# Optimization experiments

Hardware: AMD Instinct MI355X
Metric: run time of the kernel (lower is better)

## Reference

```python
import math
import jax, jax.numpy as jnp
import numpy as np

B, S, D, H = 2, 2048, 1024, 16
HD = D // H  # head_dim = 64
LN_EPS = 1e-5


def setup_inputs() -> dict:
    key = jax.random.key(0)
    ks = jax.random.split(key, 12)
    scale = 1.0 / math.sqrt(D)
    inp = {
        "x": jax.random.normal(ks[0], (B, S, D), dtype=jnp.float32),
        "cdr_mask": jax.random.uniform(ks[1], (B, 1, S, S), dtype=jnp.float32),
        "Wq": jax.random.normal(ks[2], (D, D), dtype=jnp.float32) * scale,
        "bq": jnp.zeros((D,), dtype=jnp.float32),
        "Wk": jax.random.normal(ks[3], (D, D), dtype=jnp.float32) * scale,
        "bk": jnp.zeros((D,), dtype=jnp.float32),
        "Wv": jax.random.normal(ks[4], (D, D), dtype=jnp.float32) * scale,
        "bv": jnp.zeros((D,), dtype=jnp.float32),
        "Wo": jax.random.normal(ks[5], (D, D), dtype=jnp.float32) * scale,
        "bo": jnp.zeros((D,), dtype=jnp.float32),
        "gamma": jnp.ones((D,), dtype=jnp.float32),
        "beta": jnp.zeros((D,), dtype=jnp.float32),
        "cdr_weight": jnp.float32(1.0),
    }
    return inp


def _rotate_half(t):
    # even / odd interleaved halves, as in the torch module
    t1 = t[..., ::2]
    t2 = t[..., 1::2]
    return jnp.stack((-t2, t1), axis=-1).reshape(t.shape)


def reference(x, cdr_mask, Wq, bq, Wk, bk, Wv, bv, Wo, bo, gamma, beta, cdr_weight):
    b, s, d = x.shape
    # RoPE tables (concatenated, NOT interleaved -- faithful to source)
    inv_freq = 1.0 / (10000.0 ** (jnp.arange(0, HD, 2, dtype=jnp.float32) / HD))
    pos = jnp.arange(s, dtype=jnp.float32)
    sinusoid = pos[:, None] * inv_freq[None, :]          # [S, HD/2]
    sin_pos = jnp.concatenate([jnp.sin(sinusoid)] * 2, axis=-1)[None, None]  # [1,1,S,HD]
    cos_pos = jnp.concatenate([jnp.cos(sinusoid)] * 2, axis=-1)[None, None]

    def proj(W, bias):
        return (x @ W.T + bias).reshape(b, s, H, HD).transpose(0, 2, 1, 3)  # [B,H,S,HD]

    Q = proj(Wq, bq)
    K = proj(Wk, bk)
    V = proj(Wv, bv)
    Q = Q * cos_pos + _rotate_half(Q) * sin_pos
    K = K * cos_pos + _rotate_half(K) * sin_pos

    scores = jnp.einsum('bhqd,bhkd->bhqk', Q, K) / math.sqrt(HD)
    scores = scores + cdr_mask * cdr_weight
    probs = jax.nn.softmax(scores, axis=-1)
    attn = jnp.einsum('bhqk,bhkd->bhqd', probs, V)       # [B,H,S,HD]
    attn = attn.transpose(0, 2, 1, 3).reshape(b, s, d)
    out = attn @ Wo.T + bo                               # dropout is identity at eval

    y = x + out
    mu = jnp.mean(y, axis=-1, keepdims=True)
    var = jnp.var(y, axis=-1, keepdims=True)
    return (y - mu) / jnp.sqrt(var + LN_EPS) * gamma + beta
```

## Files before the change

### kernel.cpp

```cpp
#include <hip/hip_runtime.h>
#include <hip/hip_bf16.h>
#include <math.h>

#define Bn  2
#define Sn  2048
#define Dn  1024
#define Hn  16
#define HDn 64

typedef __attribute__((ext_vector_type(8))) short bf16x8;
typedef __attribute__((ext_vector_type(4))) short bf16x4;
typedef __attribute__((ext_vector_type(4))) float f32x4;

#define LOG2E 1.44269504088896340736f

__device__ __forceinline__ float fexp2(float x) {
    return __builtin_amdgcn_exp2f(x);
}

__device__ __forceinline__ uint2 pack4bf(float a, float b, float c, float d) {
    union { __hip_bfloat162 h2[2]; uint2 u; } p;
    p.h2[0] = __float22bfloat162_rn(make_float2(a, b));
    p.h2[1] = __float22bfloat162_rn(make_float2(c, d));
    return p.u;
}

__device__ __forceinline__ bf16x4 pack4bfv(float a, float b, float c, float d) {
    union { __hip_bfloat162 h2[2]; bf16x4 v; } p;
    p.h2[0] = __float22bfloat162_rn(make_float2(a, b));
    p.h2[1] = __float22bfloat162_rn(make_float2(c, d));
    return p.v;
}

__device__ __forceinline__ void g2l16(const void* g, void* lbase) {
    __builtin_amdgcn_global_load_lds(
        (const __attribute__((address_space(1))) void*)g,
        (__attribute__((address_space(3))) void*)lbase, 16, 0, 0);
}

__global__ __launch_bounds__(256) void prep_kernel(
    const float* __restrict__ x,
    const float* __restrict__ Wq, const float* __restrict__ Wk,
    const float* __restrict__ Wv, const float* __restrict__ Wo,
    __hip_bfloat16* __restrict__ Xb,
    __hip_bfloat16* __restrict__ Wqb, __hip_bfloat16* __restrict__ Wkb,
    __hip_bfloat16* __restrict__ Wvb, __hip_bfloat16* __restrict__ Wob)
{
    const int bx = blockIdx.x, tid = threadIdx.x;
    if (bx < 4096) {
        const size_t i = (size_t)bx * 1024 + tid * 4;
        float4 v = *(const float4*)(x + i);
        *(uint2*)(Xb + i) = pack4bf(v.x, v.y, v.z, v.w);
    } else {
        const int r = bx - 4096;
        const int which = r >> 10;
        const size_t i = (size_t)(r & 1023) * 1024 + tid * 4;
        const float* s = (which == 0) ? Wq : (which == 1) ? Wk : (which == 2) ? Wv : Wo;
        __hip_bfloat16* d = (which == 0) ? Wqb : (which == 1) ? Wkb : (which == 2) ? Wvb : Wob;
        float4 v = *(const float4*)(s + i);
        *(uint2*)(d + i) = pack4bf(v.x, v.y, v.z, v.w);
    }
}

__global__ __launch_bounds__(256) void qkv_proj(
    const __hip_bfloat16* __restrict__ X,
    const __hip_bfloat16* __restrict__ Wqb, const __hip_bfloat16* __restrict__ Wkb,
    const __hip_bfloat16* __restrict__ Wvb,
    const float* __restrict__ bq, const float* __restrict__ bk,
    const float* __restrict__ bv,
    __hip_bfloat16* __restrict__ Qo, __hip_bfloat16* __restrict__ Ko,
    __hip_bfloat16* __restrict__ Vo)
{
    __shared__ __hip_bfloat16 Xs[128 * 32];
    __shared__ __hip_bfloat16 Ws[128 * 32];
    const int tid  = threadIdx.x;
    const int w    = tid >> 6, lane = tid & 63;
    const int lrow = lane & 15, lhi = lane >> 4;
    const int L    = blockIdx.x;
    const int xcd  = L & 7, slot = L >> 3;
    const int wq   = slot >> 2, ms = slot & 3;
    const int pj   = wq >> 3;
    const int n0   = (wq & 7) * 128;
    const int m0   = (xcd + 8 * ms) * 128;
    const int rm   = (w & 1) * 64;
    const int rn   = (w >> 1) * 64;
    const int srow = lane >> 2, cb = lane & 3;

    const __hip_bfloat16* Wb   = (pj == 0) ? Wqb : (pj == 1) ? Wkb : Wvb;
    const float*          bias = (pj == 0) ? bq : (pj == 1) ? bk : bv;

    f32x4 acc[16];
#pragma unroll
    for (int i = 0; i < 16; i++) acc[i] = (f32x4){0.f, 0.f, 0.f, 0.f};

    for (int k0 = 0; k0 < Dn; k0 += 32) {
#pragma unroll
        for (int j = 0; j < 2; j++) {
            const int row = w * 32 + j * 16 + srow;
            const int sc  = (cb ^ ((row >> 1) & 3)) << 3;
            g2l16(X  + (size_t)(m0 + row) * Dn + k0 + sc, &Xs[(w * 32 + j * 16) * 32]);
            g2l16(Wb + (size_t)(n0 + row) * Dn + k0 + sc, &Ws[(w * 32 + j * 16) * 32]);
        }
        __syncthreads();

        bf16x8 FX[4], FW[4];
#pragma unroll
        for (int t = 0; t < 4; t++) {
            const int ra = rm + t * 16 + lrow;
            FX[t] = *(const bf16x8*)&Xs[ra * 32 + ((lhi ^ ((ra >> 1) & 3)) << 3)];
            const int rb = rn + t * 16 + lrow;
            FW[t] = *(const bf16x8*)&Ws[rb * 32 + ((lhi ^ ((rb >> 1) & 3)) << 3)];
        }
        if (pj == 2) {
#pragma unroll
            for (int tm = 0; tm < 4; tm++)
#pragma unroll
                for (int tn = 0; tn < 4; tn++)
                    acc[tm * 4 + tn] = __builtin_amdgcn_mfma_f32_16x16x32_bf16(
                        FX[tm], FW[tn], acc[tm * 4 + tn], 0, 0, 0);
        } else {
#pragma unroll
            for (int tn = 0; tn < 4; tn++)
#pragma unroll
                for (int tm = 0; tm < 4; tm++)
                    acc[tn * 4 + tm] = __builtin_amdgcn_mfma_f32_16x16x32_bf16(
                        FW[tn], FX[tm], acc[tn * 4 + tm], 0, 0, 0);
        }
        __syncthreads();
    }

    const int h = (n0 >> 6) + (w >> 1);

    if (pj != 2) {
        __hip_bfloat16* outb = (pj == 0) ? Qo : Ko;
        const float NEG_L2C = -0.41524101186092033f;
        const float SCL = 0.125f * LOG2E;
#pragma unroll
        for (int tn = 0; tn < 4; tn++) {
            const int hd0 = tn * 16 + lhi * 4;
            const float4 b4 = *(const float4*)&bias[n0 + rn + hd0];
            const float f0 = exp2f((float)((hd0 + 0) & 31) * NEG_L2C);
            const float f1 = exp2f((float)((hd0 + 1) & 31) * NEG_L2C);
            const float f2 = exp2f((float)((hd0 + 2) & 31) * NEG_L2C);
            const float f3 = exp2f((float)((hd0 + 3) & 31) * NEG_L2C);
#pragma unroll
            for (int tm = 0; tm < 4; tm++) {
                const int m = m0 + rm + tm * 16 + lrow;
                const int s = m & (Sn - 1), bb = m >> 11;
                f32x4 a = acc[tn * 4 + tm];
                float v0 = a[0] + b4.x, v1 = a[1] + b4.y;
                float v2 = a[2] + b4.z, v3 = a[3] + b4.w;
                if (pj == 0) { v0 *= SCL; v1 *= SCL; v2 *= SCL; v3 *= SCL; }
                const float sf = (float)s;
                const float c0 = __cosf(sf * f0), c1 = __cosf(sf * f1);
                const float c2 = __cosf(sf * f2), c3 = __cosf(sf * f3);
                const float s0 = __sinf(sf * f0), s1 = __sinf(sf * f1);
                const float s2 = __sinf(sf * f2), s3 = __sinf(sf * f3);
                const float r0 = v0 * c0 - v1 * s0;
                const float r1 = v1 * c1 + v0 * s1;
                const float r2 = v2 * c2 - v3 * s2;
                const float r3 = v3 * c3 + v2 * s3;
                *(uint2*)(outb + ((size_t)(bb * Hn + h) * Sn + s) * HDn + hd0) =
                    pack4bf(r0, r1, r2, r3);
            }
        }
    } else {
#pragma unroll
        for (int tn = 0; tn < 4; tn++) {
            const int c = tn * 16 + lrow;
            const float bc = bias[n0 + rn + c];
#pragma unroll
            for (int tm = 0; tm < 4; tm++) {
                const int mb = m0 + rm + tm * 16 + lhi * 4;
                const int s = mb & (Sn - 1), bb = mb >> 11;
                f32x4 a = acc[tm * 4 + tn];
                *(uint2*)(Vo + ((size_t)(bb * Hn + h) * HDn + c) * Sn + s) =
                    pack4bf(a[0] + bc, a[1] + bc, a[2] + bc, a[3] + bc);
            }
        }
    }
}

__global__ __launch_bounds__(256) void o_proj(
    const __hip_bfloat16* __restrict__ X,
    const __hip_bfloat16* __restrict__ Wb,
    const float* __restrict__ bias,
    const float* __restrict__ resid,
    float* __restrict__ outf)
{
    __shared__ __hip_bfloat16 Xs[128 * 32];
    __shared__ __hip_bfloat16 Ws[128 * 32];
    const int tid  = threadIdx.x;
    const int w    = tid >> 6, lane = tid & 63;
    const int lrow = lane & 15, lhi = lane >> 4;
    const int L    = blockIdx.x;
    const int xcd  = L & 7, slot = L >> 3;
    const int n0   = (slot >> 2) * 128;
    const int m0   = (xcd + 8 * (slot & 3)) * 128;
    const int rm   = (w & 1) * 64;
    const int rn   = (w >> 1) * 64;
    const int srow = lane >> 2, cb = lane & 3;

    f32x4 acc[16];
#pragma unroll
    for (int i = 0; i < 16; i++) acc[i] = (f32x4){0.f, 0.f, 0.f, 0.f};

    for (int k0 = 0; k0 < Dn; k0 += 32) {
#pragma unroll
        for (int j = 0; j < 2; j++) {
            const int row = w * 32 + j * 16 + srow;
            const int sc  = (cb ^ ((row >> 1) & 3)) << 3;
            g2l16(X  + (size_t)(m0 + row) * Dn + k0 + sc, &Xs[(w * 32 + j * 16) * 32]);
            g2l16(Wb + (size_t)(n0 + row) * Dn + k0 + sc, &Ws[(w * 32 + j * 16) * 32]);
        }
        __syncthreads();

        bf16x8 FX[4], FW[4];
#pragma unroll
        for (int t = 0; t < 4; t++) {
            const int ra = rm + t * 16 + lrow;
            FX[t] = *(const bf16x8*)&Xs[ra * 32 + ((lhi ^ ((ra >> 1) & 3)) << 3)];
            const int rb = rn + t * 16 + lrow;
            FW[t] = *(const bf16x8*)&Ws[rb * 32 + ((lhi ^ ((rb >> 1) & 3)) << 3)];
        }
#pragma unroll
        for (int tn = 0; tn < 4; tn++)
#pragma unroll
            for (int tm = 0; tm < 4; tm++)
                acc[tn * 4 + tm] = __builtin_amdgcn_mfma_f32_16x16x32_bf16(
                    FW[tn], FX[tm], acc[tn * 4 + tm], 0, 0, 0);
        __syncthreads();
    }

#pragma unroll
    for (int tn = 0; tn < 4; tn++) {
        const int nb = n0 + rn + tn * 16 + lhi * 4;
        const float4 b4 = *(const float4*)&bias[nb];
#pragma unroll
        for (int tm = 0; tm < 4; tm++) {
            const int m = m0 + rm + tm * 16 + lrow;
            f32x4 a = acc[tn * 4 + tm];
            const float4 rr = *(const float4*)&resid[(size_t)m * Dn + nb];
            *(float4*)(outf + (size_t)m * Dn + nb) =
                make_float4(a[0] + b4.x + rr.x, a[1] + b4.y + rr.y,
                            a[2] + b4.z + rr.z, a[3] + b4.w + rr.w);
        }
    }
}

struct __align__(16) TileBuf {
    __hip_bfloat16 K[64 * 64];
    __hip_bfloat16 V[64 * 64];
    float          M[64 * 64];
};

__device__ __forceinline__ void stage_tiles(
    TileBuf& t,
    const __hip_bfloat16* __restrict__ Kb,
    const __hip_bfloat16* __restrict__ Vb,
    const float* __restrict__ Mq0,
    int k0, int w, int lane)
{
#pragma unroll
    for (int j = 0; j < 2; j++) {
        const int row = w * 16 + j * 8 + (lane >> 3);
        const int blk = (lane & 7) ^ (row & 7);
        g2l16(Kb + (size_t)(k0 + row) * HDn + blk * 8, &t.K[(w * 16 + j * 8) * 64]);
        g2l16(Vb + (size_t)row * Sn + k0 + blk * 8,    &t.V[(w * 16 + j * 8) * 64]);
    }
#pragma unroll
    for (int j = 0; j < 4; j++) {
        const int row = w * 16 + j * 4 + (lane >> 4);
        const int blk = (lane & 15) ^ (row & 7);
        g2l16(Mq0 + (size_t)row * Sn + k0 + blk * 4,   &t.M[(w * 16 + j * 4) * 64]);
    }
}

__global__ __launch_bounds__(256) void attn_kernel(
    const __hip_bfloat16* __restrict__ Q,
    const __hip_bfloat16* __restrict__ K,
    const __hip_bfloat16* __restrict__ Vt,
    const float* __restrict__ mask,
    const float* __restrict__ cwp,
    __hip_bfloat16* __restrict__ A)
{
    __shared__ TileBuf tb[2];
    const int tid  = threadIdx.x;
    const int w    = tid >> 6, lane = tid & 63;
    const int lrow = lane & 15, lhi = lane >> 4;
    const int L    = blockIdx.x;
    const int xcd  = L & 7, slot = L >> 3;
    const int b    = xcd >> 2;
    const int h    = (xcd & 3) * 4 + (slot & 3);
    const int q0   = (slot >> 2) * 64;
    const int bh   = b * Hn + h;
    const int q    = q0 + w * 16 + lrow;
    const float cwl = cwp[0] * LOG2E;

    const __hip_bfloat16* Qp  = Q + ((size_t)bh * Sn + q) * HDn + lhi * 8;
    const bf16x8 Qf0 = *(const bf16x8*)(Qp);
    const bf16x8 Qf1 = *(const bf16x8*)(Qp + 32);
    const __hip_bfloat16* Kb  = K  + (size_t)bh * Sn * HDn;
    const __hip_bfloat16* Vb  = Vt + (size_t)bh * HDn * Sn;
    const float*          Mq0 = mask + ((size_t)b * Sn + q0) * Sn;

    f32x4 Oc[4];
#pragma unroll
    for (int i = 0; i < 4; i++) Oc[i] = (f32x4){0.f, 0.f, 0.f, 0.f};
    float lsum = 0.f;

    stage_tiles(tb[0], Kb, Vb, Mq0, 0, w, lane);
    __syncthreads();

    for (int it = 0; it < Sn / 64; it++) {
        const int k0 = it * 64;
        if (it + 1 < Sn / 64)
            stage_tiles(tb[(it + 1) & 1], Kb, Vb, Mq0, k0 + 64, w, lane);
        const TileBuf& t = tb[it & 1];

        f32x4 st[4];
#pragma unroll
        for (int kt = 0; kt < 4; kt++) {
            const int rl = kt * 16 + lrow;
            const bf16x8 ka = *(const bf16x8*)&t.K[rl * 64 + ((lhi       ^ (rl & 7)) * 8)];
            const bf16x8 kc = *(const bf16x8*)&t.K[rl * 64 + (((4 + lhi) ^ (rl & 7)) * 8)];
            f32x4 z = (f32x4){0.f, 0.f, 0.f, 0.f};
            z = __builtin_amdgcn_mfma_f32_16x16x32_bf16(ka, Qf0, z, 0, 0, 0);
            z = __builtin_amdgcn_mfma_f32_16x16x32_bf16(kc, Qf1, z, 0, 0, 0);
            st[kt] = z;
        }

        const int rq = w * 16 + lrow;
        bf16x4 pk[4];
#pragma unroll
        for (int kt = 0; kt < 4; kt++) {
            const int mb = (kt * 4 + lhi) ^ (rq & 7);
            const f32x4 mf = *(const f32x4*)&t.M[rq * 64 + mb * 4];
            const float p0 = fexp2(fmaf(mf[0], cwl, st[kt][0]));
            const float p1 = fexp2(fmaf(mf[1], cwl, st[kt][1]));
            const float p2 = fexp2(fmaf(mf[2], cwl, st[kt][2]));
            const float p3 = fexp2(fmaf(mf[3], cwl, st[kt][3]));
            lsum += (p0 + p1) + (p2 + p3);
            pk[kt] = pack4bfv(p0, p1, p2, p3);
        }

#pragma unroll
        for (int ch = 0; ch < 4; ch++) {
            const int rv = ch * 16 + lrow;
#pragma unroll
            for (int kt = 0; kt < 4; kt++) {
                const int eo = (((2 * kt + (lhi >> 1)) ^ (rv & 7)) * 8) + (lhi & 1) * 4;
                const bf16x4 vf = *(const bf16x4*)&t.V[rv * 64 + eo];
                Oc[ch] = __builtin_amdgcn_mfma_f32_16x16x16bf16_1k(
                    vf, pk[kt], Oc[ch], 0, 0, 0);
            }
        }
        __syncthreads();
    }

    lsum += __shfl_xor(lsum, 16, 64);
    lsum += __shfl_xor(lsum, 32, 64);
    const float inv = 1.f / lsum;

    __hip_bfloat16* ap = A + ((size_t)(b * Sn + q)) * Dn + h * HDn;
#pragma unroll
    for (int ch = 0; ch < 4; ch++) {
        *(uint2*)(ap + ch * 16 + lhi * 4) =
            pack4bf(Oc[ch][0] * inv, Oc[ch][1] * inv, Oc[ch][2] * inv, Oc[ch][3] * inv);
    }
}

__global__ __launch_bounds__(256) void ln_kernel(
    const float* __restrict__ Yin, const float* __restrict__ gamma,
    const float* __restrict__ beta, float* __restrict__ out)
{
    __shared__ float2 wred[4];
    const int m   = blockIdx.x;
    const int tid = threadIdx.x;
    const size_t base = (size_t)m * Dn + tid * 4;
    float4 y = *(const float4*)(Yin + base);

    float s1 = y.x + y.y + y.z + y.w;
    float s2 = y.x * y.x + y.y * y.y + y.z * y.z + y.w * y.w;
#pragma unroll
    for (int off = 32; off; off >>= 1) {
        s1 += __shfl_xor(s1, off, 64);
        s2 += __shfl_xor(s2, off, 64);
    }
    if ((tid & 63) == 0) wred[tid >> 6] = make_float2(s1, s2);
    __syncthreads();
    const float S1 = wred[0].x + wred[1].x + wred[2].x + wred[3].x;
    const float S2 = wred[0].y + wred[1].y + wred[2].y + wred[3].y;
    const float mu  = S1 * (1.f / Dn);
    const float var = S2 * (1.f / Dn) - mu * mu;
    const float rin = rsqrtf(var + 1e-5f);

    float4 gv = *(const float4*)(gamma + tid * 4);
    float4 bv = *(const float4*)(beta  + tid * 4);
    *(float4*)(out + base) = make_float4((y.x - mu) * rin * gv.x + bv.x,
                                         (y.y - mu) * rin * gv.y + bv.y,
                                         (y.z - mu) * rin * gv.z + bv.z,
                                         (y.w - mu) * rin * gv.w + bv.w);
}

extern "C" void kernel_launch(void* const* d_in, const int* in_sizes, int n_in,
                              void* d_out, int out_size, void* d_ws, size_t ws_size,
                              hipStream_t stream)
{
    const float* x     = (const float*)d_in[0];
    const float* mask  = (const float*)d_in[1];
    const float* Wq    = (const float*)d_in[2];
    const float* bq    = (const float*)d_in[3];
    const float* Wk    = (const float*)d_in[4];
    const float* bk    = (const float*)d_in[5];
    const float* Wv    = (const float*)d_in[6];
    const float* bv    = (const float*)d_in[7];
    const float* Wo    = (const float*)d_in[8];
    const float* bo    = (const float*)d_in[9];
    const float* gamma = (const float*)d_in[10];
    const float* beta  = (const float*)d_in[11];
    const float* cw    = (const float*)d_in[12];
    float* out = (float*)d_out;

    const size_t MB = 1024 * 1024;
    char* ws = (char*)d_ws;
    __hip_bfloat16* Xb  = (__hip_bfloat16*)(ws);
    __hip_bfloat16* Qb  = (__hip_bfloat16*)(ws +  8 * MB);
    __hip_bfloat16* Kb  = (__hip_bfloat16*)(ws + 16 * MB);
    __hip_bfloat16* Vtb = (__hip_bfloat16*)(ws + 24 * MB);
    __hip_bfloat16* Wqb = (__hip_bfloat16*)(ws + 32 * MB);
    __hip_bfloat16* Wkb = (__hip_bfloat16*)(ws + 34 * MB);
    __hip_bfloat16* Wvb = (__hip_bfloat16*)(ws + 36 * MB);
    __hip_bfloat16* Wob = (__hip_bfloat16*)(ws + 38 * MB);
    __hip_bfloat16* Ab  = Xb;

    prep_kernel<<<8192, 256, 0, stream>>>(x, Wq, Wk, Wv, Wo,
                                          Xb, Wqb, Wkb, Wvb, Wob);
    qkv_proj<<<768, 256, 0, stream>>>(Xb, Wqb, Wkb, Wvb,
                                      bq, bk, bv, Qb, Kb, Vtb);
    attn_kernel<<<1024, 256, 0, stream>>>(Qb, Kb, Vtb, mask, cw, Ab);
    o_proj<<<256, 256, 0, stream>>>(Ab, Wob, bo, x, out);
    ln_kernel<<<Bn * Sn, 256, 0, stream>>>(out, gamma, beta, out);
}
```

Baseline: 282.6 us.

## Double GEMM K-tile to 64 and precompute RoPE cos/sin table

The QKV and output projection GEMMs now stage 64-wide K slices in LDS with an 8-way XOR swizzle, which halves the number of barrier pairs per tile while doubling shared memory per block. Separately, the RoPE cos/sin values are computed once into a global table by extra blocks of the prep kernel and read in the QKV epilogue, replacing per-element exp2/sin/cos. This trades transcendental math for extra global loads and a table write.

```diff
diff --git a/kernel.cpp b/kernel.cpp
--- a/kernel.cpp
+++ b/kernel.cpp
@@ -44,14 +44,15 @@
     const float* __restrict__ Wv, const float* __restrict__ Wo,
     __hip_bfloat16* __restrict__ Xb,
     __hip_bfloat16* __restrict__ Wqb, __hip_bfloat16* __restrict__ Wkb,
-    __hip_bfloat16* __restrict__ Wvb, __hip_bfloat16* __restrict__ Wob)
+    __hip_bfloat16* __restrict__ Wvb, __hip_bfloat16* __restrict__ Wob,
+    float2* __restrict__ CS)
 {
     const int bx = blockIdx.x, tid = threadIdx.x;
     if (bx < 4096) {
         const size_t i = (size_t)bx * 1024 + tid * 4;
         float4 v = *(const float4*)(x + i);
         *(uint2*)(Xb + i) = pack4bf(v.x, v.y, v.z, v.w);
-    } else {
+    } else if (bx < 8192) {
         const int r = bx - 4096;
         const int which = r >> 10;
         const size_t i = (size_t)(r & 1023) * 1024 + tid * 4;
@@ -59,6 +60,16 @@
         __hip_bfloat16* d = (which == 0) ? Wqb : (which == 1) ? Wkb : (which == 2) ? Wvb : Wob;
         float4 v = *(const float4*)(s + i);
         *(uint2*)(d + i) = pack4bf(v.x, v.y, v.z, v.w);
+    } else {
+        const float NEG_L2C = -0.41524101186092033f;
+        const int idx = ((bx - 8192) * 256 + tid) * 2;
+        const int s = idx >> 6, d0 = idx & 63;
+        const float sf = (float)s;
+        const float f0 = exp2f((float)(d0 & 31) * NEG_L2C);
+        const float f1 = exp2f((float)((d0 + 1) & 31) * NEG_L2C);
+        *(float4*)(&CS[(size_t)s * 64 + d0]) =
+            make_float4(__cosf(sf * f0), __sinf(sf * f0),
+                        __cosf(sf * f1), __sinf(sf * f1));
     }
 }
 
@@ -68,11 +79,12 @@
     const __hip_bfloat16* __restrict__ Wvb,
     const float* __restrict__ bq, const float* __restrict__ bk,
     const float* __restrict__ bv,
+    const float2* __restrict__ CS,
     __hip_bfloat16* __restrict__ Qo, __hip_bfloat16* __restrict__ Ko,
     __hip_bfloat16* __restrict__ Vo)
 {
-    __shared__ __hip_bfloat16 Xs[128 * 32];
-    __shared__ __hip_bfloat16 Ws[128 * 32];
+    __shared__ __hip_bfloat16 Xs[128 * 64];
+    __shared__ __hip_bfloat16 Ws[128 * 64];
     const int tid  = threadIdx.x;
     const int w    = tid >> 6, lane = tid & 63;
     const int lrow = lane & 15, lhi = lane >> 4;
@@ -84,7 +96,7 @@
     const int m0   = (xcd + 8 * ms) * 128;
     const int rm   = (w & 1) * 64;
     const int rn   = (w >> 1) * 64;
-    const int srow = lane >> 2, cb = lane & 3;
+    const int srow = lane >> 3, scb = lane & 7;
 
     const __hip_bfloat16* Wb   = (pj == 0) ? Wqb : (pj == 1) ? Wkb : Wvb;
     const float*          bias = (pj == 0) ? bq : (pj == 1) ? bk : bv;
@@ -93,38 +105,41 @@
 #pragma unroll
     for (int i = 0; i < 16; i++) acc[i] = (f32x4){0.f, 0.f, 0.f, 0.f};
 
-    for (int k0 = 0; k0 < Dn; k0 += 32) {
-#pragma unroll
-        for (int j = 0; j < 2; j++) {
-            const int row = w * 32 + j * 16 + srow;
-            const int sc  = (cb ^ ((row >> 1) & 3)) << 3;
-            g2l16(X  + (size_t)(m0 + row) * Dn + k0 + sc, &Xs[(w * 32 + j * 16) * 32]);
-            g2l16(Wb + (size_t)(n0 + row) * Dn + k0 + sc, &Ws[(w * 32 + j * 16) * 32]);
+    for (int k0 = 0; k0 < Dn; k0 += 64) {
+#pragma unroll
+        for (int j = 0; j < 4; j++) {
+            const int row = w * 32 + j * 8 + srow;
+            const int sc  = ((scb ^ (row & 7)) << 3);
+            g2l16(X  + (size_t)(m0 + row) * Dn + k0 + sc, &Xs[(w * 32 + j * 8) * 64]);
+            g2l16(Wb + (size_t)(n0 + row) * Dn + k0 + sc, &Ws[(w * 32 + j * 8) * 64]);
         }
         __syncthreads();
 
-        bf16x8 FX[4], FW[4];
-#pragma unroll
-        for (int t = 0; t < 4; t++) {
-            const int ra = rm + t * 16 + lrow;
-            FX[t] = *(const bf16x8*)&Xs[ra * 32 + ((lhi ^ ((ra >> 1) & 3)) << 3)];
-            const int rb = rn + t * 16 + lrow;
-            FW[t] = *(const bf16x8*)&Ws[rb * 32 + ((lhi ^ ((rb >> 1) & 3)) << 3)];
-        }
-        if (pj == 2) {
-#pragma unroll
-            for (int tm = 0; tm < 4; tm++)
+#pragma unroll
+        for (int ksub = 0; ksub < 2; ksub++) {
+            bf16x8 FX[4], FW[4];
+#pragma unroll
+            for (int t = 0; t < 4; t++) {
+                const int ra = rm + t * 16 + lrow;
+                FX[t] = *(const bf16x8*)&Xs[ra * 64 + (((ksub * 4 + lhi) ^ (ra & 7)) << 3)];
+                const int rb = rn + t * 16 + lrow;
+                FW[t] = *(const bf16x8*)&Ws[rb * 64 + (((ksub * 4 + lhi) ^ (rb & 7)) << 3)];
+            }
+            if (pj == 2) {
+#pragma unroll
+                for (int tm = 0; tm < 4; tm++)
+#pragma unroll
+                    for (int tn = 0; tn < 4; tn++)
+                        acc[tm * 4 + tn] = __builtin_amdgcn_mfma_f32_16x16x32_bf16(
+                            FX[tm], FW[tn], acc[tm * 4 + tn], 0, 0, 0);
+            } else {
 #pragma unroll
                 for (int tn = 0; tn < 4; tn++)
-                    acc[tm * 4 + tn] = __builtin_amdgcn_mfma_f32_16x16x32_bf16(
-                        FX[tm], FW[tn], acc[tm * 4 + tn], 0, 0, 0);
-        } else {
-#pragma unroll
-            for (int tn = 0; tn < 4; tn++)
-#pragma unroll
-                for (int tm = 0; tm < 4; tm++)
-                    acc[tn * 4 + tm] = __builtin_amdgcn_mfma_f32_16x16x32_bf16(
-                        FW[tn], FX[tm], acc[tn * 4 + tm], 0, 0, 0);
+#pragma unroll
+                    for (int tm = 0; tm < 4; tm++)
+                        acc[tn * 4 + tm] = __builtin_amdgcn_mfma_f32_16x16x32_bf16(
+                            FW[tn], FX[tm], acc[tn * 4 + tm], 0, 0, 0);
+            }
         }
         __syncthreads();
     }
@@ -133,16 +148,11 @@
 
     if (pj != 2) {
         __hip_bfloat16* outb = (pj == 0) ? Qo : Ko;
-        const float NEG_L2C = -0.41524101186092033f;
         const float SCL = 0.125f * LOG2E;
 #pragma unroll
         for (int tn = 0; tn < 4; tn++) {
             const int hd0 = tn * 16 + lhi * 4;
             const float4 b4 = *(const float4*)&bias[n0 + rn + hd0];
-            const float f0 = exp2f((float)((hd0 + 0) & 31) * NEG_L2C);
-            const float f1 = exp2f((float)((hd0 + 1) & 31) * NEG_L2C);
-            const float f2 = exp2f((float)((hd0 + 2) & 31) * NEG_L2C);
-            const float f3 = exp2f((float)((hd0 + 3) & 31) * NEG_L2C);
 #pragma unroll
             for (int tm = 0; tm < 4; tm++) {
                 const int m = m0 + rm + tm * 16 + lrow;
@@ -151,15 +161,12 @@
                 float v0 = a[0] + b4.x, v1 = a[1] + b4.y;
                 float v2 = a[2] + b4.z, v3 = a[3] + b4.w;
                 if (pj == 0) { v0 *= SCL; v1 *= SCL; v2 *= SCL; v3 *= SCL; }
-                const float sf = (float)s;
-                const float c0 = __cosf(sf * f0), c1 = __cosf(sf * f1);
-                const float c2 = __cosf(sf * f2), c3 = __cosf(sf * f3);
-                const float s0 = __sinf(sf * f0), s1 = __sinf(sf * f1);
-                const float s2 = __sinf(sf * f2), s3 = __sinf(sf * f3);
-                const float r0 = v0 * c0 - v1 * s0;
-                const float r1 = v1 * c1 + v0 * s1;
-                const float r2 = v2 * c2 - v3 * s2;
-                const float r3 = v3 * c3 + v2 * s3;
+                const float4 cs01 = *(const float4*)&CS[(size_t)s * 64 + hd0];
+                const float4 cs23 = *(const float4*)&CS[(size_t)s * 64 + hd0 + 2];
+                const float r0 = v0 * cs01.x - v1 * cs01.y;
+                const float r1 = v1 * cs01.z + v0 * cs01.w;
+                const float r2 = v2 * cs23.x - v3 * cs23.y;
+                const float r3 = v3 * cs23.z + v2 * cs23.w;
                 *(uint2*)(outb + ((size_t)(bb * Hn + h) * Sn + s) * HDn + hd0) =
                     pack4bf(r0, r1, r2, r3);
             }
@@ -188,8 +195,8 @@
     const float* __restrict__ resid,
     float* __restrict__ outf)
 {
-    __shared__ __hip_bfloat16 Xs[128 * 32];
-    __shared__ __hip_bfloat16 Ws[128 * 32];
+    __shared__ __hip_bfloat16 Xs[128 * 64];
+    __shared__ __hip_bfloat16 Ws[128 * 64];
     const int tid  = threadIdx.x;
     const int w    = tid >> 6, lane = tid & 63;
     const int lrow = lane & 15, lhi = lane >> 4;
@@ -199,36 +206,39 @@
     const int m0   = (xcd + 8 * (slot & 3)) * 128;
     const int rm   = (w & 1) * 64;
     const int rn   = (w >> 1) * 64;
-    const int srow = lane >> 2, cb = lane & 3;
+    const int srow = lane >> 3, scb = lane & 7;
 
     f32x4 acc[16];
 #pragma unroll
     for (int i = 0; i < 16; i++) acc[i] = (f32x4){0.f, 0.f, 0.f, 0.f};
 
-    for (int k0 = 0; k0 < Dn; k0 += 32) {
-#pragma unroll
-        for (int j = 0; j < 2; j++) {
-            const int row = w * 32 + j * 16 + srow;
-            const int sc  = (cb ^ ((row >> 1) & 3)) << 3;
-            g2l16(X  + (size_t)(m0 + row) * Dn + k0 + sc, &Xs[(w * 32 + j * 16) * 32]);
-            g2l16(Wb + (size_t)(n0 + row) * Dn + k0 + sc, &Ws[(w * 32 + j * 16) * 32]);
+    for (int k0 = 0; k0 < Dn; k0 += 64) {
+#pragma unroll
+        for (int j = 0; j < 4; j++) {
+            const int row = w * 32 + j * 8 + srow;
+            const int sc  = ((scb ^ (row & 7)) << 3);
+            g2l16(X  + (size_t)(m0 + row) * Dn + k0 + sc, &Xs[(w * 32 + j * 8) * 64]);
+            g2l16(Wb + (size_t)(n0 + row) * Dn + k0 + sc, &Ws[(w * 32 + j * 8) * 64]);
         }
         __syncthreads();
 
-        bf16x8 FX[4], FW[4];
-#pragma unroll
-        for (int t = 0; t < 4; t++) {
-            const int ra = rm + t * 16 + lrow;
-            FX[t] = *(const bf16x8*)&Xs[ra * 32 + ((lhi ^ ((ra >> 1) & 3)) << 3)];
-            const int rb = rn + t * 16 + lrow;
-            FW[t] = *(const bf16x8*)&Ws[rb * 32 + ((lhi ^ ((rb >> 1) & 3)) << 3)];
-        }
-#pragma unroll
-        for (int tn = 0; tn < 4; tn++)
-#pragma unroll
-            for (int tm = 0; tm < 4; tm++)
-                acc[tn * 4 + tm] = __builtin_amdgcn_mfma_f32_16x16x32_bf16(
-                    FW[tn], FX[tm], acc[tn * 4 + tm], 0, 0, 0);
+#pragma unroll
+        for (int ksub = 0; ksub < 2; ksub++) {
+            bf16x8 FX[4], FW[4];
+#pragma unroll
+            for (int t = 0; t < 4; t++) {
+                const int ra = rm + t * 16 + lrow;
+                FX[t] = *(const bf16x8*)&Xs[ra * 64 + (((ksub * 4 + lhi) ^ (ra & 7)) << 3)];
+                const int rb = rn + t * 16 + lrow;
+                FW[t] = *(const bf16x8*)&Ws[rb * 64 + (((ksub * 4 + lhi) ^ (rb & 7)) << 3)];
+            }
+#pragma unroll
+            for (int tn = 0; tn < 4; tn++)
+#pragma unroll
+                for (int tm = 0; tm < 4; tm++)
+                    acc[tn * 4 + tm] = __builtin_amdgcn_mfma_f32_16x16x32_bf16(
+                        FW[tn], FX[tm], acc[tn * 4 + tm], 0, 0, 0);
+        }
         __syncthreads();
     }
 
@@ -432,12 +442,13 @@
     __hip_bfloat16* Wkb = (__hip_bfloat16*)(ws + 34 * MB);
     __hip_bfloat16* Wvb = (__hip_bfloat16*)(ws + 36 * MB);
     __hip_bfloat16* Wob = (__hip_bfloat16*)(ws + 38 * MB);
+    float2*         CS  = (float2*)        (ws + 40 * MB);
     __hip_bfloat16* Ab  = Xb;
 
-    prep_kernel<<<8192, 256, 0, stream>>>(x, Wq, Wk, Wv, Wo,
-                                          Xb, Wqb, Wkb, Wvb, Wob);
+    prep_kernel<<<8448, 256, 0, stream>>>(x, Wq, Wk, Wv, Wo,
+                                          Xb, Wqb, Wkb, Wvb, Wob, CS);
     qkv_proj<<<768, 256, 0, stream>>>(Xb, Wqb, Wkb, Wvb,
-                                      bq, bk, bv, Qb, Kb, Vtb);
+                                      bq, bk, bv, CS, Qb, Kb, Vtb);
     attn_kernel<<<1024, 256, 0, stream>>>(Qb, Kb, Vtb, mask, cw, Ab);
     o_proj<<<256, 256, 0, stream>>>(Ab, Wob, bo, x, out);
     ln_kernel<<<Bn * Sn, 256, 0, stream>>>(out, gamma, beta, out);
```

Measured after the change: 283.9 us. Within noise of the previous version (+0.5%).
